# Performance work log

Hardware: AMD Instinct MI355X
Metric: run time of the kernel (lower is better)

## Reference

```python
import jax, jax.numpy as jnp
import numpy as np

EPS = 1e-12  # torch F.normalize eps


def setup_inputs() -> dict:
    key = jax.random.key(0)
    k1, k2, k3 = jax.random.split(key, 3)
    N, C, H, W = 64, 512, 30, 30
    K = 64
    x = jax.random.normal(k1, (N, C, H, W), dtype=jnp.float32)
    conv_w = jax.random.normal(k2, (K, C), dtype=jnp.float32) * 0.02
    centroids = jax.random.uniform(k3, (K, C), dtype=jnp.float32)
    return {"x": x, "conv_w": conv_w, "centroids": centroids}


def reference(x, conv_w, centroids):
    N, C, H, W = x.shape
    K = conv_w.shape[0]
    # descriptor-wise L2 normalization over channel dim (torch F.normalize, p=2, dim=1)
    norm = jnp.sqrt(jnp.sum(x * x, axis=1, keepdims=True))
    x = x / jnp.maximum(norm, EPS)
    xf = x.reshape(N, C, H * W)  # [N, C, P]
    # 1x1 conv (no bias) -> logits [N, K, P]; softmax over clusters K
    logits = jnp.einsum("ncp,kc->nkp", xf, conv_w)
    a = jax.nn.softmax(logits, axis=1)  # [N, K, P]
    # vlad[n,k,c] = sum_p a[n,k,p] * (x[n,c,p] - centroids[k,c])
    #            = (a @ x^T)[n,k,c] - centroids[k,c] * sum_p a[n,k,p]
    vlad = jnp.einsum("nkp,ncp->nkc", a, xf) - a.sum(axis=-1)[:, :, None] * centroids[None]
    return vlad
```

## Files before the change

### kernel.cpp

```cpp
#include <hip/hip_runtime.h>

typedef __attribute__((ext_vector_type(8))) __bf16 bf16x8;
typedef __attribute__((ext_vector_type(4))) __bf16 bf16x4;
typedef __attribute__((ext_vector_type(4))) float f32x4;

#define LGKM_BAR() do { asm volatile("s_waitcnt lgkmcnt(0)" ::: "memory"); \
                        __builtin_amdgcn_s_barrier(); } while (0)

namespace {
constexpr int N_ = 64, C_ = 512, P_ = 900, K_ = 64;
constexpr int PP = 960;
constexpr size_t TOT_X = (size_t)N_ * C_ * P_;
constexpr size_t AT_BYTES  = (size_t)N_ * K_ * PP * 2;
constexpr size_t ASUM_OFF  = AT_BYTES;
constexpr size_t WB_OFF    = ASUM_OFF + (size_t)N_ * K_ * 4;
}

__global__ __launch_bounds__(256) void k_prep_w(const float* __restrict__ w,
                                                __bf16* __restrict__ wb,
                                                float* __restrict__ asum) {
  const int t = blockIdx.x * 256 + threadIdx.x;
  const int i = t * 4;
  if (i < K_ * C_) {
    float4 v = *reinterpret_cast<const float4*>(w + i);
    wb[i]   = (__bf16)v.x; wb[i+1] = (__bf16)v.y;
    wb[i+2] = (__bf16)v.z; wb[i+3] = (__bf16)v.w;
  }
  if (t < N_ * K_) asum[t] = 0.f;
}

__global__ __launch_bounds__(256) void k_phase1(const float* __restrict__ x,
                                                const __bf16* __restrict__ wb,
                                                __bf16* __restrict__ at,
                                                float* __restrict__ asum) {
  __shared__ __bf16 Xl[2][64][40];
  __shared__ float SsqP[64][5];
  __shared__ float Sw[64][5];
  const int n   = blockIdx.y;
  const int p0  = blockIdx.x * 64;
  const int tid = threadIdx.x;
  const int w   = tid >> 6, l = tid & 63;
  const int l15 = l & 15,  lh = l >> 4;

  bf16x8 afr[16];
  #pragma unroll
  for (int s = 0; s < 16; ++s)
    afr[s] = *reinterpret_cast<const bf16x8*>(
        wb + (size_t)(16 * w + l15) * C_ + s * 32 + lh * 8);

  const size_t xbase = (size_t)n * C_ * P_ + p0 + l;
  float nx[4][8];
  float sq = 0.f;
  f32x4 acc[4] = {};

  #pragma unroll
  for (int b = 0; b < 4; ++b)
    #pragma unroll
    for (int j = 0; j < 8; ++j) {
      size_t off = xbase + (size_t)(b * 32 + w * 8 + j) * P_;
      if (off > TOT_X - 1) off = TOT_X - 1;
      nx[b][j] = x[off];
    }
  {
    bf16x8 pk;
    #pragma unroll
    for (int j = 0; j < 8; ++j) { sq = fmaf(nx[0][j], nx[0][j], sq); pk[j] = (__bf16)nx[0][j]; }
    *reinterpret_cast<bf16x8*>(&Xl[0][l][w * 8]) = pk;
  }
  LGKM_BAR();

  #pragma unroll
  for (int s = 0; s < 16; ++s) {
    if (s + 4 < 16) {
      #pragma unroll
      for (int j = 0; j < 8; ++j) {
        size_t off = xbase + (size_t)((s + 4) * 32 + w * 8 + j) * P_;
        if (off > TOT_X - 1) off = TOT_X - 1;
        nx[s & 3][j] = x[off];
      }
    }
    #pragma unroll
    for (int t = 0; t < 4; ++t) {
      bf16x8 b = *reinterpret_cast<const bf16x8*>(&Xl[s & 1][16 * t + l15][lh * 8]);
      acc[t] = __builtin_amdgcn_mfma_f32_16x16x32_bf16(afr[s], b, acc[t], 0, 0, 0);
    }
    if (s < 15) {
      bf16x8 pk;
      #pragma unroll
      for (int j = 0; j < 8; ++j) {
        const float v = nx[(s + 1) & 3][j];
        sq = fmaf(v, v, sq); pk[j] = (__bf16)v;
      }
      *reinterpret_cast<bf16x8*>(&Xl[(s + 1) & 1][l][w * 8]) = pk;
      LGKM_BAR();
    }
  }

  SsqP[l][w] = sq;
  __syncthreads();

  float invn[4], invs_[4];
  bool valid[4];
  #pragma unroll
  for (int t = 0; t < 4; ++t) {
    const int pl = 16 * t + l15;
    const float ss = SsqP[pl][0] + SsqP[pl][1] + SsqP[pl][2] + SsqP[pl][3];
    invn[t] = 1.f / fmaxf(sqrtf(ss), 1e-12f);
    valid[t] = (p0 + pl) < P_;
    float ps = 0.f;
    #pragma unroll
    for (int r = 0; r < 4; ++r) {
      acc[t][r] = __expf(acc[t][r] * invn[t]);
      ps += acc[t][r];
    }
    ps += __shfl_xor(ps, 16, 64);
    ps += __shfl_xor(ps, 32, 64);
    if (lh == 0) Sw[pl][w] = ps;
  }
  __syncthreads();
  #pragma unroll
  for (int t = 0; t < 4; ++t) {
    const int pl = 16 * t + l15;
    invs_[t] = 1.f / (Sw[pl][0] + Sw[pl][1] + Sw[pl][2] + Sw[pl][3]);
  }

  #pragma unroll
  for (int t = 0; t < 4; ++t) {
    const int p = p0 + 16 * t + l15;
    #pragma unroll
    for (int r = 0; r < 4; ++r) {
      const int k = 16 * w + lh * 4 + r;
      const float ar = acc[t][r] * invs_[t];
      at[((size_t)n * K_ + k) * PP + p] = valid[t] ? (__bf16)(ar * invn[t]) : (__bf16)0.f;
    }
  }
  #pragma unroll
  for (int r = 0; r < 4; ++r) {
    float v = 0.f;
    #pragma unroll
    for (int t = 0; t < 4; ++t)
      v += valid[t] ? acc[t][r] * invs_[t] : 0.f;
    v += __shfl_xor(v, 1, 64); v += __shfl_xor(v, 2, 64);
    v += __shfl_xor(v, 4, 64); v += __shfl_xor(v, 8, 64);
    if (l15 == 0)
      unsafeAtomicAdd(asum + n * K_ + 16 * w + lh * 4 + r, v);
  }
}

__global__ __launch_bounds__(256) void k_phase2(const float* __restrict__ x,
                                                const __bf16* __restrict__ at,
                                                const float* __restrict__ asum,
                                                const float* __restrict__ cent,
                                                float* __restrict__ out) {
  __shared__ __bf16 Al[2][64][40];
  __shared__ __bf16 Xl[2][64][40];
  const int n   = blockIdx.y;
  const int c0  = blockIdx.x * 64;
  const int tid = threadIdx.x;
  const int w   = tid >> 6, l = tid & 63;
  const int l15 = l & 15,  lh = l >> 4;

  const int ak  = tid >> 2, ach = tid & 3;
  const int xc  = tid >> 3, xch = tid & 7;
  const size_t abase = ((size_t)n * K_ + ak) * PP + ach * 8;
  const size_t xbase0 = ((size_t)n * C_ + c0 + xc) * P_ + xch * 4;
  const size_t xbase1 = ((size_t)n * C_ + c0 + xc + 32) * P_ + xch * 4;

  f32x4 acc[4] = {};
  bf16x8 na; float4 v0, v1;

  auto LOAD = [&](int s) {
    na = *reinterpret_cast<const bf16x8*>(at + abase + s * 32);
    size_t o0 = xbase0 + s * 32; if (o0 > TOT_X - 4) o0 = TOT_X - 4;
    size_t o1 = xbase1 + s * 32; if (o1 > TOT_X - 4) o1 = TOT_X - 4;
    v0 = *reinterpret_cast<const float4*>(x + o0);
    v1 = *reinterpret_cast<const float4*>(x + o1);
  };
  auto STORE = [&](int b) {
    *reinterpret_cast<bf16x8*>(&Al[b][ak][ach * 8]) = na;
    bf16x4 p0 = { (__bf16)v0.x, (__bf16)v0.y, (__bf16)v0.z, (__bf16)v0.w };
    bf16x4 p1 = { (__bf16)v1.x, (__bf16)v1.y, (__bf16)v1.z, (__bf16)v1.w };
    *reinterpret_cast<bf16x4*>(&Xl[b][xc][xch * 4])      = p0;
    *reinterpret_cast<bf16x4*>(&Xl[b][xc + 32][xch * 4]) = p1;
  };

  LOAD(0); STORE(0);
  LGKM_BAR();

  #pragma unroll 2
  for (int s = 0; s < 29; ++s) {
    if (s < 28) LOAD(s + 1);
    bf16x8 b = *reinterpret_cast<const bf16x8*>(&Xl[s & 1][16 * w + l15][lh * 8]);
    #pragma unroll
    for (int m = 0; m < 4; ++m) {
      bf16x8 a = *reinterpret_cast<const bf16x8*>(&Al[s & 1][16 * m + l15][lh * 8]);
      acc[m] = __builtin_amdgcn_mfma_f32_16x16x32_bf16(a, b, acc[m], 0, 0, 0);
    }
    if (s < 28) STORE((s + 1) & 1);
    LGKM_BAR();
  }

  const int c = c0 + 16 * w + l15;
  #pragma unroll
  for (int m = 0; m < 4; ++m) {
    #pragma unroll
    for (int r = 0; r < 4; ++r) {
      const int k = 16 * m + lh * 4 + r;
      out[((size_t)n * K_ + k) * C_ + c] =
          acc[m][r] - asum[n * K_ + k] * cent[(size_t)k * C_ + c];
    }
  }
}

extern "C" void kernel_launch(void* const* d_in, const int* in_sizes, int n_in,
                              void* d_out, int out_size, void* d_ws, size_t ws_size,
                              hipStream_t stream) {
  const float* x    = (const float*)d_in[0];
  const float* w    = (const float*)d_in[1];
  const float* cent = (const float*)d_in[2];
  float* out = (float*)d_out;
  char* wsb  = (char*)d_ws;
  __bf16* at   = (__bf16*)wsb;
  float*  asum = (float*)(wsb + ASUM_OFF);
  __bf16* wb   = (__bf16*)(wsb + WB_OFF);

  k_prep_w<<<dim3(32), dim3(256), 0, stream>>>(w, wb, asum);
  k_phase1<<<dim3(15, 64), dim3(256), 0, stream>>>(x, wb, at, asum);
  k_phase2<<<dim3(8, 64), dim3(256), 0, stream>>>(x, at, asum, cent, out);
}
```

Before: 70.55 us.

## Pre-transpose x to bf16 pixel-major layout and simplify phase1 to LDS-free MFMA

Adds a conversion kernel that transposes x into a bf16 [n][p][c] workspace buffer. Phase1 then loads contiguous channel rows per pixel directly from global memory into MFMA operands, with no shared memory staging or barriers. The softmax and norm reductions become wave-local shuffles because each wave now owns 16 pixels and all 64 clusters. In exchange it adds a full extra pass over x (fp32 read plus bf16 write), and the norm is now computed from bf16-rounded values.

```diff
diff --git a/kernel.cpp b/kernel.cpp
--- a/kernel.cpp
+++ b/kernel.cpp
@@ -11,9 +11,10 @@
 constexpr int N_ = 64, C_ = 512, P_ = 900, K_ = 64;
 constexpr int PP = 960;
 constexpr size_t TOT_X = (size_t)N_ * C_ * P_;
-constexpr size_t AT_BYTES  = (size_t)N_ * K_ * PP * 2;
-constexpr size_t ASUM_OFF  = AT_BYTES;
-constexpr size_t WB_OFF    = ASUM_OFF + (size_t)N_ * K_ * 4;
+constexpr size_t AT_BYTES = (size_t)N_ * K_ * PP * 2;
+constexpr size_t ASUM_OFF = AT_BYTES;
+constexpr size_t WB_OFF   = ASUM_OFF + (size_t)N_ * K_ * 4;
+constexpr size_t XT_OFF   = 8388608;
 }
 
 __global__ __launch_bounds__(256) void k_prep_w(const float* __restrict__ w,
@@ -29,122 +30,94 @@
   if (t < N_ * K_) asum[t] = 0.f;
 }
 
-__global__ __launch_bounds__(256) void k_phase1(const float* __restrict__ x,
+__global__ __launch_bounds__(256) void k_convert(const float* __restrict__ x,
+                                                 __bf16* __restrict__ xt) {
+  __shared__ float T[64][65];
+  const int n = blockIdx.z, c0 = blockIdx.y * 64, p0 = blockIdx.x * 64;
+  const int tid = threadIdx.x;
+  const int cr = tid >> 4, pq = (tid & 15) * 4;
+  #pragma unroll
+  for (int i = 0; i < 4; ++i) {
+    const int c = cr + i * 16;
+    float4 v = make_float4(0.f, 0.f, 0.f, 0.f);
+    if (p0 + pq < P_)
+      v = *reinterpret_cast<const float4*>(
+          x + ((size_t)n * C_ + c0 + c) * P_ + p0 + pq);
+    *reinterpret_cast<float4*>(&T[c][pq]) = v;
+  }
+  __syncthreads();
+  const int pr = tid >> 2, cs = (tid & 3) * 16;
+  bf16x8 o0, o1;
+  #pragma unroll
+  for (int j = 0; j < 8; ++j) o0[j] = (__bf16)T[cs + j][pr];
+  #pragma unroll
+  for (int j = 0; j < 8; ++j) o1[j] = (__bf16)T[cs + 8 + j][pr];
+  __bf16* dst = xt + ((size_t)n * PP + p0 + pr) * C_ + c0 + cs;
+  *reinterpret_cast<bf16x8*>(dst)     = o0;
+  *reinterpret_cast<bf16x8*>(dst + 8) = o1;
+}
+
+__global__ __launch_bounds__(256) void k_phase1(const __bf16* __restrict__ xt,
                                                 const __bf16* __restrict__ wb,
                                                 __bf16* __restrict__ at,
                                                 float* __restrict__ asum) {
-  __shared__ __bf16 Xl[2][64][40];
-  __shared__ float SsqP[64][5];
-  __shared__ float Sw[64][5];
   const int n   = blockIdx.y;
-  const int p0  = blockIdx.x * 64;
   const int tid = threadIdx.x;
   const int w   = tid >> 6, l = tid & 63;
   const int l15 = l & 15,  lh = l >> 4;
-
-  bf16x8 afr[16];
-  #pragma unroll
-  for (int s = 0; s < 16; ++s)
-    afr[s] = *reinterpret_cast<const bf16x8*>(
-        wb + (size_t)(16 * w + l15) * C_ + s * 32 + lh * 8);
-
-  const size_t xbase = (size_t)n * C_ * P_ + p0 + l;
-  float nx[4][8];
+  const int p   = blockIdx.x * 64 + w * 16 + l15;
+  const __bf16* xrow  = xt + ((size_t)n * PP + p) * C_ + lh * 8;
+  const __bf16* wbase = wb + (size_t)l15 * C_ + lh * 8;
+
+  f32x4 acc[4] = {};
   float sq = 0.f;
-  f32x4 acc[4] = {};
-
-  #pragma unroll
-  for (int b = 0; b < 4; ++b)
-    #pragma unroll
-    for (int j = 0; j < 8; ++j) {
-      size_t off = xbase + (size_t)(b * 32 + w * 8 + j) * P_;
-      if (off > TOT_X - 1) off = TOT_X - 1;
-      nx[b][j] = x[off];
-    }
-  {
-    bf16x8 pk;
-    #pragma unroll
-    for (int j = 0; j < 8; ++j) { sq = fmaf(nx[0][j], nx[0][j], sq); pk[j] = (__bf16)nx[0][j]; }
-    *reinterpret_cast<bf16x8*>(&Xl[0][l][w * 8]) = pk;
-  }
-  LGKM_BAR();
-
   #pragma unroll
   for (int s = 0; s < 16; ++s) {
-    if (s + 4 < 16) {
-      #pragma unroll
-      for (int j = 0; j < 8; ++j) {
-        size_t off = xbase + (size_t)((s + 4) * 32 + w * 8 + j) * P_;
-        if (off > TOT_X - 1) off = TOT_X - 1;
-        nx[s & 3][j] = x[off];
-      }
-    }
-    #pragma unroll
-    for (int t = 0; t < 4; ++t) {
-      bf16x8 b = *reinterpret_cast<const bf16x8*>(&Xl[s & 1][16 * t + l15][lh * 8]);
-      acc[t] = __builtin_amdgcn_mfma_f32_16x16x32_bf16(afr[s], b, acc[t], 0, 0, 0);
-    }
-    if (s < 15) {
-      bf16x8 pk;
-      #pragma unroll
-      for (int j = 0; j < 8; ++j) {
-        const float v = nx[(s + 1) & 3][j];
-        sq = fmaf(v, v, sq); pk[j] = (__bf16)v;
-      }
-      *reinterpret_cast<bf16x8*>(&Xl[(s + 1) & 1][l][w * 8]) = pk;
-      LGKM_BAR();
-    }
-  }
-
-  SsqP[l][w] = sq;
-  __syncthreads();
-
-  float invn[4], invs_[4];
-  bool valid[4];
-  #pragma unroll
-  for (int t = 0; t < 4; ++t) {
-    const int pl = 16 * t + l15;
-    const float ss = SsqP[pl][0] + SsqP[pl][1] + SsqP[pl][2] + SsqP[pl][3];
-    invn[t] = 1.f / fmaxf(sqrtf(ss), 1e-12f);
-    valid[t] = (p0 + pl) < P_;
-    float ps = 0.f;
-    #pragma unroll
-    for (int r = 0; r < 4; ++r) {
-      acc[t][r] = __expf(acc[t][r] * invn[t]);
-      ps += acc[t][r];
-    }
-    ps += __shfl_xor(ps, 16, 64);
-    ps += __shfl_xor(ps, 32, 64);
-    if (lh == 0) Sw[pl][w] = ps;
-  }
-  __syncthreads();
-  #pragma unroll
-  for (int t = 0; t < 4; ++t) {
-    const int pl = 16 * t + l15;
-    invs_[t] = 1.f / (Sw[pl][0] + Sw[pl][1] + Sw[pl][2] + Sw[pl][3]);
-  }
-
-  #pragma unroll
-  for (int t = 0; t < 4; ++t) {
-    const int p = p0 + 16 * t + l15;
-    #pragma unroll
-    for (int r = 0; r < 4; ++r) {
-      const int k = 16 * w + lh * 4 + r;
-      const float ar = acc[t][r] * invs_[t];
-      at[((size_t)n * K_ + k) * PP + p] = valid[t] ? (__bf16)(ar * invn[t]) : (__bf16)0.f;
-    }
-  }
-  #pragma unroll
-  for (int r = 0; r < 4; ++r) {
-    float v = 0.f;
-    #pragma unroll
-    for (int t = 0; t < 4; ++t)
-      v += valid[t] ? acc[t][r] * invs_[t] : 0.f;
-    v += __shfl_xor(v, 1, 64); v += __shfl_xor(v, 2, 64);
-    v += __shfl_xor(v, 4, 64); v += __shfl_xor(v, 8, 64);
-    if (l15 == 0)
-      unsafeAtomicAdd(asum + n * K_ + 16 * w + lh * 4 + r, v);
-  }
+    bf16x8 b = *reinterpret_cast<const bf16x8*>(xrow + s * 32);
+    #pragma unroll
+    for (int j = 0; j < 8; ++j) { const float f = (float)b[j]; sq = fmaf(f, f, sq); }
+    #pragma unroll
+    for (int m = 0; m < 4; ++m) {
+      bf16x8 a = *reinterpret_cast<const bf16x8*>(wbase + (size_t)m * 16 * C_ + s * 32);
+      acc[m] = __builtin_amdgcn_mfma_f32_16x16x32_bf16(a, b, acc[m], 0, 0, 0);
+    }
+  }
+  sq += __shfl_xor(sq, 16, 64);
+  sq += __shfl_xor(sq, 32, 64);
+  const float invn = 1.f / fmaxf(sqrtf(sq), 1e-12f);
+  const bool  valid = p < P_;
+
+  float ps = 0.f;
+  #pragma unroll
+  for (int m = 0; m < 4; ++m)
+    #pragma unroll
+    for (int r = 0; r < 4; ++r) {
+      acc[m][r] = __expf(acc[m][r] * invn);
+      ps += acc[m][r];
+    }
+  ps += __shfl_xor(ps, 16, 64);
+  ps += __shfl_xor(ps, 32, 64);
+  const float invs = 1.f / ps;
+  const float sc   = invs * invn;
+
+  #pragma unroll
+  for (int m = 0; m < 4; ++m)
+    #pragma unroll
+    for (int r = 0; r < 4; ++r) {
+      const int k = 16 * m + lh * 4 + r;
+      at[((size_t)n * K_ + k) * PP + p] =
+          valid ? (__bf16)(acc[m][r] * sc) : (__bf16)0.f;
+    }
+  #pragma unroll
+  for (int m = 0; m < 4; ++m)
+    #pragma unroll
+    for (int r = 0; r < 4; ++r) {
+      float v = valid ? acc[m][r] * invs : 0.f;
+      v += __shfl_xor(v, 1, 64); v += __shfl_xor(v, 2, 64);
+      v += __shfl_xor(v, 4, 64); v += __shfl_xor(v, 8, 64);
+      if (l15 == 0)
+        unsafeAtomicAdd(asum + n * K_ + 16 * m + lh * 4 + r, v);
+    }
 }
 
 __global__ __launch_bounds__(256) void k_phase2(const float* __restrict__ x,
@@ -162,7 +135,7 @@
 
   const int ak  = tid >> 2, ach = tid & 3;
   const int xc  = tid >> 3, xch = tid & 7;
-  const size_t abase = ((size_t)n * K_ + ak) * PP + ach * 8;
+  const size_t abase  = ((size_t)n * K_ + ak) * PP + ach * 8;
   const size_t xbase0 = ((size_t)n * C_ + c0 + xc) * P_ + xch * 4;
   const size_t xbase1 = ((size_t)n * C_ + c0 + xc + 32) * P_ + xch * 4;
 
@@ -223,8 +196,10 @@
   __bf16* at   = (__bf16*)wsb;
   float*  asum = (float*)(wsb + ASUM_OFF);
   __bf16* wb   = (__bf16*)(wsb + WB_OFF);
+  __bf16* xt   = (__bf16*)(wsb + XT_OFF);
 
   k_prep_w<<<dim3(32), dim3(256), 0, stream>>>(w, wb, asum);
-  k_phase1<<<dim3(15, 64), dim3(256), 0, stream>>>(x, wb, at, asum);
+  k_convert<<<dim3(15, 8, 64), dim3(256), 0, stream>>>(x, xt);
+  k_phase1<<<dim3(15, 64), dim3(256), 0, stream>>>(xt, wb, at, asum);
   k_phase2<<<dim3(8, 64), dim3(256), 0, stream>>>(x, at, asum, cent, out);
 }
```

Measured after the change: 122.8 us. 1.74x slower.

## Compute per-pixel sum of squares in a separate vectorized kernel

Applied to the files above, without the earlier changes.

Moves the channel-wise sum-of-squares computation out of the phase1 GEMM loop into a new kernel that reads x with float4 loads and accumulates partial sums per 64-channel chunk via atomics into a global buffer. Phase1 then reads the precomputed norms instead of doing FMAs and an LDS reduction. This adds an extra full pass over x (about 118 MB) and another launch, trading memory traffic for a lighter phase1 inner loop.

```diff
diff --git a/kernel.cpp b/kernel.cpp
--- a/kernel.cpp
+++ b/kernel.cpp
@@ -1,4 +1,5 @@
 #include <hip/hip_runtime.h>
+#include <stdint.h>
 
 typedef __attribute__((ext_vector_type(8))) __bf16 bf16x8;
 typedef __attribute__((ext_vector_type(4))) __bf16 bf16x4;
@@ -11,14 +12,16 @@
 constexpr int N_ = 64, C_ = 512, P_ = 900, K_ = 64;
 constexpr int PP = 960;
 constexpr size_t TOT_X = (size_t)N_ * C_ * P_;
-constexpr size_t AT_BYTES  = (size_t)N_ * K_ * PP * 2;
-constexpr size_t ASUM_OFF  = AT_BYTES;
-constexpr size_t WB_OFF    = ASUM_OFF + (size_t)N_ * K_ * 4;
+constexpr size_t AT_BYTES = (size_t)N_ * K_ * PP * 2;
+constexpr size_t ASUM_OFF = AT_BYTES;
+constexpr size_t WB_OFF   = ASUM_OFF + (size_t)N_ * K_ * 4;
+constexpr size_t SSQ_OFF  = WB_OFF + (size_t)K_ * C_ * 2 + 64;
 }
 
 __global__ __launch_bounds__(256) void k_prep_w(const float* __restrict__ w,
                                                 __bf16* __restrict__ wb,
-                                                float* __restrict__ asum) {
+                                                float* __restrict__ asum,
+                                                float* __restrict__ gssq) {
   const int t = blockIdx.x * 256 + threadIdx.x;
   const int i = t * 4;
   if (i < K_ * C_) {
@@ -27,14 +30,37 @@
     wb[i+2] = (__bf16)v.z; wb[i+3] = (__bf16)v.w;
   }
   if (t < N_ * K_) asum[t] = 0.f;
+  #pragma unroll
+  for (int j = 0; j < 8; ++j) {
+    const int idx = t * 8 + j;
+    if (idx < N_ * PP) gssq[idx] = 0.f;
+  }
+}
+
+__global__ __launch_bounds__(256) void k_ssq(const float* __restrict__ x,
+                                             float* __restrict__ gssq) {
+  const int cc = blockIdx.x, n = blockIdx.y;
+  const int tid = threadIdx.x;
+  if (tid >= 225) return;
+  const float* xb = x + ((size_t)n * C_ + cc * 64) * P_ + tid * 4;
+  float4 sq = make_float4(0.f, 0.f, 0.f, 0.f);
+  #pragma unroll 8
+  for (int c = 0; c < 64; ++c) {
+    const float4 v = *reinterpret_cast<const float4*>(xb + (size_t)c * P_);
+    sq.x = fmaf(v.x, v.x, sq.x); sq.y = fmaf(v.y, v.y, sq.y);
+    sq.z = fmaf(v.z, v.z, sq.z); sq.w = fmaf(v.w, v.w, sq.w);
+  }
+  float* o = gssq + (size_t)n * PP + tid * 4;
+  unsafeAtomicAdd(o + 0, sq.x); unsafeAtomicAdd(o + 1, sq.y);
+  unsafeAtomicAdd(o + 2, sq.z); unsafeAtomicAdd(o + 3, sq.w);
 }
 
 __global__ __launch_bounds__(256) void k_phase1(const float* __restrict__ x,
                                                 const __bf16* __restrict__ wb,
+                                                const float* __restrict__ gssq,
                                                 __bf16* __restrict__ at,
                                                 float* __restrict__ asum) {
   __shared__ __bf16 Xl[2][64][40];
-  __shared__ float SsqP[64][5];
   __shared__ float Sw[64][5];
   const int n   = blockIdx.y;
   const int p0  = blockIdx.x * 64;
@@ -50,7 +76,6 @@
 
   const size_t xbase = (size_t)n * C_ * P_ + p0 + l;
   float nx[4][8];
-  float sq = 0.f;
   f32x4 acc[4] = {};
 
   #pragma unroll
@@ -64,7 +89,7 @@
   {
     bf16x8 pk;
     #pragma unroll
-    for (int j = 0; j < 8; ++j) { sq = fmaf(nx[0][j], nx[0][j], sq); pk[j] = (__bf16)nx[0][j]; }
+    for (int j = 0; j < 8; ++j) pk[j] = (__bf16)nx[0][j];
     *reinterpret_cast<bf16x8*>(&Xl[0][l][w * 8]) = pk;
   }
   LGKM_BAR();
@@ -87,26 +112,20 @@
     if (s < 15) {
       bf16x8 pk;
       #pragma unroll
-      for (int j = 0; j < 8; ++j) {
-        const float v = nx[(s + 1) & 3][j];
-        sq = fmaf(v, v, sq); pk[j] = (__bf16)v;
-      }
+      for (int j = 0; j < 8; ++j) pk[j] = (__bf16)nx[(s + 1) & 3][j];
       *reinterpret_cast<bf16x8*>(&Xl[(s + 1) & 1][l][w * 8]) = pk;
       LGKM_BAR();
     }
   }
 
-  SsqP[l][w] = sq;
-  __syncthreads();
-
   float invn[4], invs_[4];
   bool valid[4];
   #pragma unroll
   for (int t = 0; t < 4; ++t) {
     const int pl = 16 * t + l15;
-    const float ss = SsqP[pl][0] + SsqP[pl][1] + SsqP[pl][2] + SsqP[pl][3];
-    invn[t] = 1.f / fmaxf(sqrtf(ss), 1e-12f);
     valid[t] = (p0 + pl) < P_;
+    const float ss = valid[t] ? gssq[(size_t)n * PP + p0 + pl] : 0.f;
+    invn[t] = valid[t] ? (1.f / fmaxf(sqrtf(ss), 1e-12f)) : 0.f;
     float ps = 0.f;
     #pragma unroll
     for (int r = 0; r < 4; ++r) {
@@ -162,7 +181,7 @@
 
   const int ak  = tid >> 2, ach = tid & 3;
   const int xc  = tid >> 3, xch = tid & 7;
-  const size_t abase = ((size_t)n * K_ + ak) * PP + ach * 8;
+  const size_t abase  = ((size_t)n * K_ + ak) * PP + ach * 8;
   const size_t xbase0 = ((size_t)n * C_ + c0 + xc) * P_ + xch * 4;
   const size_t xbase1 = ((size_t)n * C_ + c0 + xc + 32) * P_ + xch * 4;
 
@@ -223,8 +242,10 @@
   __bf16* at   = (__bf16*)wsb;
   float*  asum = (float*)(wsb + ASUM_OFF);
   __bf16* wb   = (__bf16*)(wsb + WB_OFF);
-
-  k_prep_w<<<dim3(32), dim3(256), 0, stream>>>(w, wb, asum);
-  k_phase1<<<dim3(15, 64), dim3(256), 0, stream>>>(x, wb, at, asum);
+  float*  gssq = (float*)(wsb + SSQ_OFF);
+
+  k_prep_w<<<dim3(32), dim3(256), 0, stream>>>(w, wb, asum, gssq);
+  k_ssq<<<dim3(8, 64), dim3(256), 0, stream>>>(x, gssq);
+  k_phase1<<<dim3(15, 64), dim3(256), 0, stream>>>(x, wb, gssq, at, asum);
   k_phase2<<<dim3(8, 64), dim3(256), 0, stream>>>(x, at, asum, cent, out);
 }
```

Measured after the change: 91.71 us. +30.0%, slower.
